# Kernel tuning notes

Hardware: AMD Instinct MI355X
Metric: run time of the kernel (lower is better)

Reference implementation:

```python
import jax, jax.numpy as jnp
import numpy as np

SEQ, D_IN, D_OUT, RANK, N_ADAPTERS = 8192, 4096, 4096, 16, 8


def setup_inputs() -> dict:
    key = jax.random.key(0)
    ks = jax.random.split(key, 7)
    return {
        "x": jax.random.normal(ks[0], (SEQ, D_IN), jnp.float32),
        "weight": jax.random.normal(ks[1], (D_IN, D_OUT), jnp.float32) * (D_IN ** -0.5),
        "bias": jax.random.normal(ks[2], (D_OUT,), jnp.float32),
        "A_buffer": jax.random.normal(ks[3], (N_ADAPTERS, RANK, D_IN), jnp.float32) * (D_IN ** -0.5),
        "B_buffer": jax.random.normal(ks[4], (N_ADAPTERS, D_OUT, RANK), jnp.float32) * (RANK ** -0.5),
        "scalings": jax.random.uniform(ks[5], (SEQ,), jnp.float32, 0.5, 2.0),
        "token_indices": jax.random.randint(ks[6], (SEQ,), 0, N_ADAPTERS, jnp.int32),
    }


def reference(x, weight, bias, A_buffer, B_buffer, scalings, token_indices):
    # Base linear layer: [S, D_in] @ [D_in, D_out] + bias
    base_output = x @ weight + bias
    n_adapters = A_buffer.shape[0]
    delta = jnp.zeros_like(base_output)
    # Grouped LoRA GEMM: per-adapter small GEMMs, masked scatter back per token.
    for e in range(n_adapters):
        # run_lora_a_gemm: x @ A[e]^T with per-token scaling -> [S, rank]
        a_out = (x @ A_buffer[e].T) * scalings[:, None]
        # run_lora_b_gemm: a_out @ B[e]^T -> [S, D_out]
        b_out = a_out @ B_buffer[e].T
        delta = delta + jnp.where((token_indices == e)[:, None], b_out, 0.0)
    return base_output + delta
```

## Files before the change

### kernel.cpp

```cpp
#include <hip/hip_runtime.h>
#include <hip/hip_bf16.h>
#include <cstdint>

#define SEQ   8192
#define DIN   4096
#define DOUT  4096
#define RANK  16
#define NAD   8
#define KC    (DIN + NAD*RANK)

using f32x4  = __attribute__((ext_vector_type(4))) float;
using bf16x8 = __attribute__((ext_vector_type(8))) short;

__device__ __forceinline__ unsigned short f2bf(float f) {
  union { float f; uint32_t u; } v; v.f = f;
  return (unsigned short)((v.u + 0x7fffu + ((v.u >> 16) & 1u)) >> 16);
}

__device__ __forceinline__ void async_copy16(void* lds, const void* gmem) {
  __builtin_amdgcn_global_load_lds(
      (__attribute__((address_space(1))) void*)(uintptr_t)gmem,
      (__attribute__((address_space(3))) void*)(uint32_t)(uintptr_t)lds,
      16, 0, 0);
}


__global__ void cvt_xa_kernel(const float* __restrict__ x, unsigned short* __restrict__ xcat,
                              const float* __restrict__ a, unsigned short* __restrict__ abf) {
  if (blockIdx.x < 4096) {
    const int64_t nchunks = (int64_t)SEQ * DIN / 8;
    for (int64_t c = (int64_t)blockIdx.x * 256 + threadIdx.x; c < nchunks;
         c += (int64_t)4096 * 256) {
      int64_t base = c * 8;
      int s = (int)(base >> 12);
      int k = (int)(base & (DIN - 1));
      float4 p = *(const float4*)(x + base);
      float4 q = *(const float4*)(x + base + 4);
      union { unsigned short h[8]; int4 v; } o;
      o.h[0]=f2bf(p.x); o.h[1]=f2bf(p.y); o.h[2]=f2bf(p.z); o.h[3]=f2bf(p.w);
      o.h[4]=f2bf(q.x); o.h[5]=f2bf(q.y); o.h[6]=f2bf(q.z); o.h[7]=f2bf(q.w);
      *(int4*)(xcat + (int64_t)s * KC + k) = o.v;
    }
  } else {
    int c = (blockIdx.x - 4096) * 256 + threadIdx.x;
    int64_t base = (int64_t)c * 8;
    float4 p = *(const float4*)(a + base);
    float4 q = *(const float4*)(a + base + 4);
    union { unsigned short h[8]; int4 v; } o;
    o.h[0]=f2bf(p.x); o.h[1]=f2bf(p.y); o.h[2]=f2bf(p.z); o.h[3]=f2bf(p.w);
    o.h[4]=f2bf(q.x); o.h[5]=f2bf(q.y); o.h[6]=f2bf(q.z); o.h[7]=f2bf(q.w);
    *(int4*)(abf + base) = o.v;
  }
}

__global__ void cvt_wb_kernel(const float* __restrict__ w, unsigned short* __restrict__ wcat,
                              const float* __restrict__ Bbuf) {
  if (blockIdx.x < 8192) {
    int t  = threadIdx.x;
    int bn = blockIdx.x & 127;
    int bk = blockIdx.x >> 7;
    int n = bn * 32 + (t & 31);
    int k = bk * 64 + (t >> 5) * 8;
    union { unsigned short h[8]; int4 v; } o;
#pragma unroll
    for (int j = 0; j < 8; j++)
      o.h[j] = f2bf(w[(int64_t)(k + j) * DOUT + n]);
    *(int4*)(wcat + (int64_t)n * KC + k) = o.v;
  } else {
    int idx = (blockIdx.x - 8192) * 256 + threadIdx.x;
    int n = idx >> 7, er = idx & 127;
    int e = er >> 4, r = er & 15;
    float v = Bbuf[((int64_t)e * DOUT + n) * RANK + r];
    wcat[(int64_t)n * KC + DIN + er] = f2bf(v);
  }
}

__global__ __launch_bounds__(256) void gemm_lora_a2(
    const unsigned short* __restrict__ A,
    const unsigned short* __restrict__ Bb,
    const float* __restrict__ scal,
    const int* __restrict__ tok,
    unsigned short* __restrict__ xcat) {
  constexpr int BK = 64;
  __shared__ unsigned short sA[2][16 * BK];
  __shared__ unsigned short sB[2][128 * BK];
  int tid = threadIdx.x, wave = tid >> 6, lane = tid & 63;
  int quad = lane >> 4, l16 = lane & 15;
  int row0 = blockIdx.x * 16;
  int f8 = l16 & 7;

  f32x4 acc[2];
  acc[0] = f32x4{0.f, 0.f, 0.f, 0.f};
  acc[1] = f32x4{0.f, 0.f, 0.f, 0.f};

  auto stage = [&](int b, int kt) {
    int k0 = kt * BK;
    if (tid < 128) {
      int r = tid >> 3, kc = ((tid & 7) ^ (r & 7)) * 8;
      async_copy16(&sA[b][tid * 8], A + (int64_t)(row0 + r) * KC + k0 + kc);
    }
#pragma unroll
    for (int i = 0; i < 4; i++) {
      int c = i * 256 + tid;
      int r = c >> 3, kc = ((c & 7) ^ (r & 7)) * 8;
      async_copy16(&sB[b][c * 8], Bb + (int64_t)r * DIN + k0 + kc);
    }
  };

  stage(0, 0);
  __syncthreads();

  for (int kt = 0; kt < DIN / BK; ++kt) {
    int cur = kt & 1;
    if (kt + 1 < DIN / BK) stage(cur ^ 1, kt + 1);
    const unsigned short* sAc = sA[cur];
    const unsigned short* sBc = sB[cur];
#pragma unroll
    for (int ks = 0; ks < 2; ks++) {
      int qp = ((ks * 4 + quad) ^ f8) * 8;
      bf16x8 af = *(const bf16x8*)&sAc[l16 * BK + qp];
      bf16x8 b0 = *(const bf16x8*)&sBc[(wave * 32 + l16) * BK + qp];
      bf16x8 b1 = *(const bf16x8*)&sBc[(wave * 32 + 16 + l16) * BK + qp];
      acc[0] = __builtin_amdgcn_mfma_f32_16x16x32_bf16(af, b0, acc[0], 0, 0, 0);
      acc[1] = __builtin_amdgcn_mfma_f32_16x16x32_bf16(af, b1, acc[1], 0, 0, 0);
    }
    __syncthreads();
  }

#pragma unroll
  for (int ni = 0; ni < 2; ni++) {
    int er = wave * 32 + ni * 16 + l16;
    int e = er >> 4;
#pragma unroll
    for (int r = 0; r < 4; r++) {
      int s = row0 + quad * 4 + r;
      float v = acc[ni][r] * scal[s];
      v = (e == tok[s]) ? v : 0.0f;
      xcat[(int64_t)s * KC + DIN + er] = f2bf(v);
    }
  }
}


#define CFENCE asm volatile("" ::: "memory")

template<int MQ>
__device__ __forceinline__ void ldsA(const unsigned short* aT, int wm, int l16, int quad,
                                     bf16x8 (&af)[4][2]) {
  int f8 = l16 & 7;
#pragma unroll
  for (int ks = 0; ks < 2; ks++) {
    int qp = ((ks * 4 + quad) ^ f8) * 8;
#pragma unroll
    for (int mi = 0; mi < 4; mi++)
      af[mi][ks] = *(const bf16x8*)&aT[(wm * 128 + MQ * 64 + mi * 16 + l16) * 64 + qp];
  }
}

template<int NQ>
__device__ __forceinline__ void ldsB(const unsigned short* bT, int wn, int l16, int quad,
                                     bf16x8 (&bq)[2][2]) {
  int f8 = l16 & 7;
#pragma unroll
  for (int ks = 0; ks < 2; ks++) {
    int qp = ((ks * 4 + quad) ^ f8) * 8;
#pragma unroll
    for (int ni = 0; ni < 2; ni++)
      bq[ni][ks] = *(const bf16x8*)&bT[(wn * 64 + NQ * 32 + ni * 16 + l16) * 64 + qp];
  }
}

template<int MQ, int NQ>
__device__ __forceinline__ void mfma_quad(f32x4 (&acc)[8][4], bf16x8 (&af)[4][2],
                                          bf16x8 (&bq)[2][2]) {
  __builtin_amdgcn_s_setprio(1);
#pragma unroll
  for (int mi = 0; mi < 4; mi++)
#pragma unroll
    for (int ni = 0; ni < 2; ni++)
#pragma unroll
      for (int ks = 0; ks < 2; ks++)
        acc[MQ * 4 + mi][NQ * 2 + ni] = __builtin_amdgcn_mfma_f32_16x16x32_bf16(
            af[mi][ks], bq[ni][ks], acc[MQ * 4 + mi][NQ * 2 + ni], 0, 0, 0);
  __builtin_amdgcn_s_setprio(0);
}

__device__ __forceinline__ void stage_A(unsigned short* sAb, const unsigned short* Ag,
                                        int mq, int k0, int tid) {
  int rr  = tid >> 3;
  int q8  = (tid & 7) * 8;
  int qc8 = ((tid & 7) ^ (rr & 7)) * 8;
  int r0 = mq * 64 + rr;
  async_copy16(sAb + r0 * 64 + q8, Ag + (int64_t)r0 * KC + k0 + qc8);
  int r1 = r0 + 128;
  async_copy16(sAb + r1 * 64 + q8, Ag + (int64_t)r1 * KC + k0 + qc8);
}

__device__ __forceinline__ void stage_B(unsigned short* sBb, const unsigned short* Bg,
                                        int nq, int k0, int tid) {
  int rB  = ((tid >> 3) & 31) | ((tid >> 8) << 6);
  int q8  = (tid & 7) * 8;
  int qc8 = ((tid & 7) ^ ((tid >> 3) & 7)) * 8;
  int r0 = nq * 32 + rB;
  async_copy16(sBb + r0 * 64 + q8, Bg + (int64_t)r0 * KC + k0 + qc8);
  int r1 = r0 + 128;
  async_copy16(sBb + r1 * 64 + q8, Bg + (int64_t)r1 * KC + k0 + qc8);
}

#define MIDBAR                                                    \
  CFENCE; __builtin_amdgcn_s_barrier();                           \
  asm volatile("s_waitcnt lgkmcnt(0)" ::: "memory")
#define ENDBAR  CFENCE; __builtin_amdgcn_s_barrier(); CFENCE

#define TILE(aT, bT, S0, S1, S2, S3, BND)                         \
  ldsA<0>(aT, wm, l16, quad, af);                                 \
  ldsB<0>(bT, wn, l16, quad, bf0);                                \
  S0; MIDBAR;                                                     \
  mfma_quad<0, 0>(acc, af, bf0);                                  \
  ENDBAR;                                                         \
  ldsB<1>(bT, wn, l16, quad, bf1);                                \
  S1; MIDBAR;                                                     \
  mfma_quad<0, 1>(acc, af, bf1);                                  \
  ENDBAR;                                                         \
  ldsA<1>(aT, wm, l16, quad, af);                                 \
  S2; MIDBAR;                                                     \
  mfma_quad<1, 1>(acc, af, bf1);                                  \
  ENDBAR;                                                         \
  S3; CFENCE;                                                     \
  mfma_quad<1, 0>(acc, af, bf0);                                  \
  BND;                                                            \
  ENDBAR

__global__ __launch_bounds__(512, 2) void gemm_main8(
    const unsigned short* __restrict__ A,
    const unsigned short* __restrict__ B,
    const float* __restrict__ bias,
    float* __restrict__ out) {
  extern __shared__ unsigned short smem[];
  unsigned short* a0 = smem;
  unsigned short* b0 = smem + 16384;
  unsigned short* a1 = smem + 32768;
  unsigned short* b1 = smem + 49152;

  int tid = threadIdx.x, wave = tid >> 6, lane = tid & 63;
  int quad = lane >> 4, l16 = lane & 15;
  int wm = wave >> 2, wn = wave & 3;

  int bid = blockIdx.x;
  int cid = (bid & 7) * 64 + (bid >> 3);
  int bm = cid >> 4, bn = cid & 15;
  int row0 = bm * 256, col0 = bn * 256;

  const unsigned short* Ag = A + (int64_t)row0 * KC;
  const unsigned short* Bg = B + (int64_t)col0 * KC;

  const f32x4 zero = {0.f, 0.f, 0.f, 0.f};
  f32x4 acc[8][4];
#pragma unroll
  for (int i = 0; i < 8; i++)
#pragma unroll
    for (int j = 0; j < 4; j++) acc[i][j] = zero;

  bf16x8 af[4][2], bf0[2][2], bf1[2][2];

  stage_A(a0, Ag, 0, 0, tid);
  stage_B(b0, Bg, 0, 0, tid);
  stage_B(b0, Bg, 1, 0, tid);
  stage_A(a0, Ag, 1, 0, tid);
  stage_A(a1, Ag, 0, 64, tid);
  stage_B(b1, Bg, 1, 64, tid);
  stage_A(a1, Ag, 1, 64, tid);
  asm volatile("s_waitcnt vmcnt(6)" ::: "memory");
  ENDBAR;

#define BND6 asm volatile("s_waitcnt vmcnt(6)" ::: "memory")

  for (int tp = 0; tp < 32; ++tp) {
    int kE = tp * 128;
    TILE(a0, b0,
         stage_B(b1, Bg, 0, kE + 64,  tid),
         stage_A(a0, Ag, 0, kE + 128, tid),
         stage_B(b0, Bg, 1, kE + 128, tid),
         stage_A(a0, Ag, 1, kE + 128, tid),
         BND6);
    TILE(a1, b1,
         stage_B(b0, Bg, 0, kE + 128, tid),
         stage_A(a1, Ag, 0, kE + 192, tid),
         stage_B(b1, Bg, 1, kE + 192, tid),
         stage_A(a1, Ag, 1, kE + 192, tid),
         BND6);
  }

  TILE(a0, b0,
       stage_B(b1, Bg, 0, 4160, tid),
       (void)0, (void)0, (void)0,
       asm volatile("s_waitcnt vmcnt(0)" ::: "memory"));

  ldsA<0>(a1, wm, l16, quad, af);
  ldsB<0>(b1, wn, l16, quad, bf0);
  mfma_quad<0, 0>(acc, af, bf0);
  ldsB<1>(b1, wn, l16, quad, bf1);
  mfma_quad<0, 1>(acc, af, bf1);
  ldsA<1>(a1, wm, l16, quad, af);
  mfma_quad<1, 1>(acc, af, bf1);
  mfma_quad<1, 0>(acc, af, bf0);

#pragma unroll
  for (int ni = 0; ni < 4; ni++) {
    int col = col0 + wn * 64 + ni * 16 + l16;
    float bv = bias[col];
#pragma unroll
    for (int mi = 0; mi < 8; mi++) {
      int rbase = row0 + wm * 128 + mi * 16 + quad * 4;
#pragma unroll
      for (int r = 0; r < 4; r++)
        out[(int64_t)(rbase + r) * DOUT + col] = acc[mi][ni][r] + bv;
    }
  }
}

__global__ void fb_aout(const float* __restrict__ x, const float* __restrict__ Abuf,
                        const float* __restrict__ scal, const int* __restrict__ tok,
                        float* __restrict__ aout) {
  int s = blockIdx.x;
  int e = tok[s];
  __shared__ float red[256];
  for (int r = 0; r < RANK; ++r) {
    float p = 0.f;
    for (int k = threadIdx.x; k < DIN; k += 256)
      p += x[(int64_t)s * DIN + k] * Abuf[((int64_t)e * RANK + r) * DIN + k];
    red[threadIdx.x] = p;
    __syncthreads();
    for (int off = 128; off > 0; off >>= 1) {
      if (threadIdx.x < off) red[threadIdx.x] += red[threadIdx.x + off];
      __syncthreads();
    }
    if (threadIdx.x == 0) aout[s * RANK + r] = red[0] * scal[s];
    __syncthreads();
  }
}
__global__ void fb_out(const float* __restrict__ x, const float* __restrict__ w,
                       const float* __restrict__ bias, const float* __restrict__ Bbuf,
                       const int* __restrict__ tok, const float* __restrict__ aout,
                       float* __restrict__ out) {
  int64_t idx = (int64_t)blockIdx.x * blockDim.x + threadIdx.x;
  int s = (int)(idx >> 12), n = (int)(idx & (DOUT - 1));
  float accv = bias[n];
  for (int k = 0; k < DIN; ++k)
    accv += x[(int64_t)s * DIN + k] * w[(int64_t)k * DOUT + n];
  int e = tok[s];
  float d = 0.f;
  for (int r = 0; r < RANK; ++r)
    d += aout[s * RANK + r] * Bbuf[((int64_t)e * DOUT + n) * RANK + r];
  out[idx] = accv + d;
}

extern "C" void kernel_launch(void* const* d_in, const int* in_sizes, int n_in,
                              void* d_out, int out_size, void* d_ws, size_t ws_size,
                              hipStream_t stream) {
  const float* x    = (const float*)d_in[0];
  const float* w    = (const float*)d_in[1];
  const float* bias = (const float*)d_in[2];
  const float* Abuf = (const float*)d_in[3];
  const float* Bbuf = (const float*)d_in[4];
  const float* scal = (const float*)d_in[5];
  const int*   tok  = (const int*)d_in[6];
  float* out = (float*)d_out;

  const size_t xcat_b = (size_t)SEQ * KC * 2;
  const size_t wcat_b = (size_t)DOUT * KC * 2;
  const size_t abf_b  = (size_t)NAD * RANK * DIN * 2;

  if (ws_size >= xcat_b + wcat_b + abf_b) {
    static bool lds_attr_done = false;
    if (!lds_attr_done) {
      (void)hipFuncSetAttribute((const void*)gemm_main8,
                                hipFuncAttributeMaxDynamicSharedMemorySize, 131072);
      lds_attr_done = true;
    }
    unsigned short* xcat = (unsigned short*)d_ws;
    unsigned short* wcat = (unsigned short*)((char*)d_ws + xcat_b);
    unsigned short* abf  = (unsigned short*)((char*)d_ws + xcat_b + wcat_b);
    cvt_xa_kernel<<<4352, 256, 0, stream>>>(x, xcat, Abuf, abf);
    cvt_wb_kernel<<<10240, 256, 0, stream>>>(w, wcat, Bbuf);
    gemm_lora_a2<<<512, 256, 0, stream>>>(xcat, abf, scal, tok, xcat);
    gemm_main8<<<512, 512, 131072, stream>>>(xcat, wcat, bias, out);
  } else {
    float* aout = (float*)d_ws;
    fb_aout<<<SEQ, 256, 0, stream>>>(x, Abuf, scal, tok, aout);
    fb_out<<<(int)(((int64_t)SEQ * DOUT) / 256), 256, 0, stream>>>(x, w, bias, Bbuf, tok, aout, out);
  }
}
```

Before: 551.8 us.

## Transpose weight via LDS tiles and double-buffer A fragments in main GEMM

The weight fp32-to-bf16 transpose now stages 64x64 tiles in shared memory. Global reads along n and global writes along k can then both be contiguous, replacing the old per-thread strided gather. The main GEMM tile schedule gains a second A-fragment register set (afA/afB), so LDS reads for the next sub-step are issued before the MFMAs of the current one. This also drops the explicit lgkmcnt waits at the mid barriers. The cost is more VGPRs under a 2-blocks-per-CU launch bound, and it leans on the compiler to insert correct LDS waits.

```diff
diff --git a/kernel.cpp b/kernel.cpp
--- a/kernel.cpp
+++ b/kernel.cpp
@@ -55,19 +55,31 @@
 
 __global__ void cvt_wb_kernel(const float* __restrict__ w, unsigned short* __restrict__ wcat,
                               const float* __restrict__ Bbuf) {
-  if (blockIdx.x < 8192) {
-    int t  = threadIdx.x;
-    int bn = blockIdx.x & 127;
-    int bk = blockIdx.x >> 7;
-    int n = bn * 32 + (t & 31);
-    int k = bk * 64 + (t >> 5) * 8;
-    union { unsigned short h[8]; int4 v; } o;
-#pragma unroll
-    for (int j = 0; j < 8; j++)
-      o.h[j] = f2bf(w[(int64_t)(k + j) * DOUT + n]);
-    *(int4*)(wcat + (int64_t)n * KC + k) = o.v;
+  if (blockIdx.x < 4096) {
+    __shared__ unsigned short tls[64 * 68];
+    int tt = threadIdx.x;
+    int n0 = (blockIdx.x & 63) * 64;
+    int k0 = (blockIdx.x >> 6) * 64;
+#pragma unroll
+    for (int j = 0; j < 8; j++) {
+      int idx = j * 256 + tt;
+      int kk = (idx >> 6) * 2;
+      int nn = idx & 63;
+      unsigned int lo = f2bf(w[(int64_t)(k0 + kk)     * DOUT + n0 + nn]);
+      unsigned int hi = f2bf(w[(int64_t)(k0 + kk + 1) * DOUT + n0 + nn]);
+      *(unsigned int*)&tls[nn * 68 + kk] = lo | (hi << 16);
+    }
+    __syncthreads();
+#pragma unroll
+    for (int pp = 0; pp < 4; pp++) {
+      int flat = pp * 256 + tt;
+      int nn = flat >> 4;
+      int kk4 = (flat & 15) * 4;
+      uint2 v = *(const uint2*)&tls[nn * 68 + kk4];
+      *(uint2*)(wcat + (int64_t)(n0 + nn) * KC + k0 + kk4) = v;
+    }
   } else {
-    int idx = (blockIdx.x - 8192) * 256 + threadIdx.x;
+    int idx = (blockIdx.x - 4096) * 256 + threadIdx.x;
     int n = idx >> 7, er = idx & 127;
     int e = er >> 4, r = er & 15;
     float v = Bbuf[((int64_t)e * DOUT + n) * RANK + r];
@@ -207,29 +219,26 @@
   async_copy16(sBb + r1 * 64 + q8, Bg + (int64_t)r1 * KC + k0 + qc8);
 }
 
-#define MIDBAR                                                    \
-  CFENCE; __builtin_amdgcn_s_barrier();                           \
-  asm volatile("s_waitcnt lgkmcnt(0)" ::: "memory")
-#define ENDBAR  CFENCE; __builtin_amdgcn_s_barrier(); CFENCE
+#define BAR  CFENCE; __builtin_amdgcn_s_barrier(); CFENCE
 
 #define TILE(aT, bT, S0, S1, S2, S3, BND)                         \
-  ldsA<0>(aT, wm, l16, quad, af);                                 \
+  ldsA<0>(aT, wm, l16, quad, afA);                                \
   ldsB<0>(bT, wn, l16, quad, bf0);                                \
-  S0; MIDBAR;                                                     \
-  mfma_quad<0, 0>(acc, af, bf0);                                  \
-  ENDBAR;                                                         \
+  S0; BAR;                                                        \
   ldsB<1>(bT, wn, l16, quad, bf1);                                \
-  S1; MIDBAR;                                                     \
-  mfma_quad<0, 1>(acc, af, bf1);                                  \
-  ENDBAR;                                                         \
-  ldsA<1>(aT, wm, l16, quad, af);                                 \
-  S2; MIDBAR;                                                     \
-  mfma_quad<1, 1>(acc, af, bf1);                                  \
-  ENDBAR;                                                         \
-  S3; CFENCE;                                                     \
-  mfma_quad<1, 0>(acc, af, bf0);                                  \
+  mfma_quad<0, 0>(acc, afA, bf0);                                 \
+  BAR;                                                            \
+  S1; BAR;                                                        \
+  ldsA<1>(aT, wm, l16, quad, afB);                                \
+  mfma_quad<0, 1>(acc, afA, bf1);                                 \
+  BAR;                                                            \
+  S2; BAR;                                                        \
+  mfma_quad<1, 1>(acc, afB, bf1);                                 \
+  BAR;                                                            \
+  S3;                                                             \
+  mfma_quad<1, 0>(acc, afB, bf0);                                 \
   BND;                                                            \
-  ENDBAR
+  BAR
 
 __global__ __launch_bounds__(512, 2) void gemm_main8(
     const unsigned short* __restrict__ A,
@@ -261,7 +270,7 @@
 #pragma unroll
     for (int j = 0; j < 4; j++) acc[i][j] = zero;
 
-  bf16x8 af[4][2], bf0[2][2], bf1[2][2];
+  bf16x8 afA[4][2], afB[4][2], bf0[2][2], bf1[2][2];
 
   stage_A(a0, Ag, 0, 0, tid);
   stage_B(b0, Bg, 0, 0, tid);
@@ -271,7 +280,7 @@
   stage_B(b1, Bg, 1, 64, tid);
   stage_A(a1, Ag, 1, 64, tid);
   asm volatile("s_waitcnt vmcnt(6)" ::: "memory");
-  ENDBAR;
+  BAR;
 
 #define BND6 asm volatile("s_waitcnt vmcnt(6)" ::: "memory")
 
@@ -296,14 +305,14 @@
        (void)0, (void)0, (void)0,
        asm volatile("s_waitcnt vmcnt(0)" ::: "memory"));
 
-  ldsA<0>(a1, wm, l16, quad, af);
+  ldsA<0>(a1, wm, l16, quad, afA);
   ldsB<0>(b1, wn, l16, quad, bf0);
-  mfma_quad<0, 0>(acc, af, bf0);
+  mfma_quad<0, 0>(acc, afA, bf0);
   ldsB<1>(b1, wn, l16, quad, bf1);
-  mfma_quad<0, 1>(acc, af, bf1);
-  ldsA<1>(a1, wm, l16, quad, af);
-  mfma_quad<1, 1>(acc, af, bf1);
-  mfma_quad<1, 0>(acc, af, bf0);
+  mfma_quad<0, 1>(acc, afA, bf1);
+  ldsA<1>(a1, wm, l16, quad, afB);
+  mfma_quad<1, 1>(acc, afB, bf1);
+  mfma_quad<1, 0>(acc, afB, bf0);
 
 #pragma unroll
   for (int ni = 0; ni < 4; ni++) {
@@ -382,7 +391,7 @@
     unsigned short* wcat = (unsigned short*)((char*)d_ws + xcat_b);
     unsigned short* abf  = (unsigned short*)((char*)d_ws + xcat_b + wcat_b);
     cvt_xa_kernel<<<4352, 256, 0, stream>>>(x, xcat, Abuf, abf);
-    cvt_wb_kernel<<<10240, 256, 0, stream>>>(w, wcat, Bbuf);
+    cvt_wb_kernel<<<6144, 256, 0, stream>>>(w, wcat, Bbuf);
     gemm_lora_a2<<<512, 256, 0, stream>>>(xcat, abf, scal, tok, xcat);
     gemm_main8<<<512, 512, 131072, stream>>>(xcat, wcat, bias, out);
   } else {
```

Result: slower. 878.9 us (+59.3%).
